# Performance work log

Hardware: AMD Instinct MI355X
Metric: run time of the kernel (lower is better)

## Reference

```python
import jax, jax.numpy as jnp
import numpy as np

DIM = 1024
HEADS = 16
HEAD_DIM = DIM // HEADS
DFF = 4 * DIM
EPS = 1e-6


def _layernorm(x, scale, bias):
    mu = jnp.mean(x, axis=-1, keepdims=True)
    var = jnp.mean(jnp.square(x - mu), axis=-1, keepdims=True)
    return (x - mu) * jax.lax.rsqrt(var + EPS) * scale + bias


def setup_inputs() -> dict:
    key = jax.random.key(0)
    ks = jax.random.split(key, 8)
    d = {}
    d["x"] = jax.random.normal(ks[0], (4, 2048, DIM), dtype=jnp.float32)
    # LayerNorm params
    d["ln1_scale"] = jnp.ones((DIM,), jnp.float32)
    d["ln1_bias"] = jnp.zeros((DIM,), jnp.float32)
    d["ln2_scale"] = jnp.ones((DIM,), jnp.float32)
    d["ln2_bias"] = jnp.zeros((DIM,), jnp.float32)
    # Attention params
    d["qkv_w"] = jax.random.normal(ks[1], (DIM, 3 * DIM), jnp.float32) * (DIM ** -0.5)
    d["qkv_b"] = jnp.zeros((3 * DIM,), jnp.float32)
    d["proj_w"] = jax.random.normal(ks[2], (DIM, DIM), jnp.float32) * (DIM ** -0.5)
    d["proj_b"] = jnp.zeros((DIM,), jnp.float32)
    # MLP params
    d["fc1_w"] = jax.random.normal(ks[3], (DIM, DFF), jnp.float32) * (DIM ** -0.5)
    d["fc1_b"] = jnp.zeros((DFF,), jnp.float32)
    d["fc2_w"] = jax.random.normal(ks[4], (DFF, DIM), jnp.float32) * (DFF ** -0.5)
    d["fc2_b"] = jnp.zeros((DIM,), jnp.float32)
    return d


def reference(x, ln1_scale, ln1_bias, ln2_scale, ln2_bias,
              qkv_w, qkv_b, proj_w, proj_b,
              fc1_w, fc1_b, fc2_w, fc2_b):
    B, S, D = x.shape
    scale = HEAD_DIM ** -0.5

    # --- Attention sub-block (pre-LN) ---
    h = _layernorm(x, ln1_scale, ln1_bias)
    qkv = h @ qkv_w + qkv_b                                  # [B,S,3D]
    qkv = qkv.reshape(B, S, 3, HEADS, HEAD_DIM)
    qkv = qkv.transpose(2, 0, 3, 1, 4)                       # [3,B,H,S,hd]
    q, k, v = qkv[0], qkv[1], qkv[2]
    attn = jnp.einsum('bhqd,bhkd->bhqk', q, k) * scale       # [B,H,S,S]
    attn = jax.nn.softmax(attn, axis=-1)
    out = jnp.einsum('bhqk,bhkd->bhqd', attn, v)             # [B,H,S,hd]
    out = out.transpose(0, 2, 1, 3).reshape(B, S, D)
    out = out @ proj_w + proj_b
    x = x + out

    # --- MLP sub-block (pre-LN) ---
    h = _layernorm(x, ln2_scale, ln2_bias)
    h = jax.nn.gelu(h @ fc1_w + fc1_b)
    h = h @ fc2_w + fc2_b
    return x + h
```

## Files before the change

kernel.cpp:

```cpp
#include <hip/hip_runtime.h>
#include <hip/hip_bf16.h>

typedef __attribute__((ext_vector_type(4))) float f32x4;
typedef __attribute__((ext_vector_type(16))) float f32x16;
typedef __attribute__((ext_vector_type(8))) short bf16x8;

__device__ __forceinline__ unsigned short f2bf(float f) {
    return __bfloat16_as_ushort(__float2bfloat16(f));
}

typedef __attribute__((address_space(1))) const unsigned char* gas_ptr;
typedef __attribute__((address_space(3))) unsigned char* las_ptr;
__device__ __forceinline__ void gload16(const void* g, void* l) {
    __builtin_amdgcn_global_load_lds((gas_ptr)g, (las_ptr)l, 16, 0, 0);
}

__device__ __forceinline__ unsigned cvt_pk_bf16(float lo, float hi) {
    unsigned r;
    asm("v_cvt_pk_bf16_f32 %0, %1, %2" : "=v"(r) : "v"(lo), "v"(hi));
    return r;
}

__global__ __launch_bounds__(256) void ln_kernel(
    const float* __restrict__ x, const float* __restrict__ scale,
    const float* __restrict__ bias, unsigned short* __restrict__ out)
{
    int row = blockIdx.x;
    const float* xr = x + (size_t)row * 1024;
    int t = threadIdx.x;
    float4 v = ((const float4*)xr)[t];
    float s  = v.x + v.y + v.z + v.w;
    float ss = v.x*v.x + v.y*v.y + v.z*v.z + v.w*v.w;
    #pragma unroll
    for (int m = 32; m; m >>= 1) { s += __shfl_down(s, m); ss += __shfl_down(ss, m); }
    __shared__ float red[8];
    int wid = t >> 6;
    if ((t & 63) == 0) { red[wid*2] = s; red[wid*2+1] = ss; }
    __syncthreads();
    s  = red[0] + red[2] + red[4] + red[6];
    ss = red[1] + red[3] + red[5] + red[7];
    float mu  = s * (1.0f/1024.0f);
    float var = ss * (1.0f/1024.0f) - mu*mu;
    float inv = rsqrtf(var + 1e-6f);
    float4 sc = ((const float4*)scale)[t];
    float4 bi = ((const float4*)bias)[t];
    ushort4 o;
    o.x = f2bf((v.x - mu)*inv*sc.x + bi.x);
    o.y = f2bf((v.y - mu)*inv*sc.y + bi.y);
    o.z = f2bf((v.z - mu)*inv*sc.z + bi.z);
    o.w = f2bf((v.w - mu)*inv*sc.w + bi.w);
    ((ushort4*)(out + (size_t)row * 1024))[t] = o;
}

__global__ __launch_bounds__(256) void transpose_kernel(
    const float* __restrict__ W, unsigned short* __restrict__ Wt, int K, int N)
{
    __shared__ float tile[32][33];
    int n0 = blockIdx.x * 32, k0 = blockIdx.y * 32;
    int tx = threadIdx.x, ty = threadIdx.y;
    #pragma unroll
    for (int j = 0; j < 32; j += 8)
        tile[ty + j][tx] = W[(size_t)(k0 + ty + j) * N + n0 + tx];
    __syncthreads();
    #pragma unroll
    for (int j = 0; j < 32; j += 8)
        Wt[(size_t)(n0 + ty + j) * K + k0 + tx] = f2bf(tile[tx][ty + j]);
}

template<int EPI>
__global__ __launch_bounds__(512, 2) void gemm256_kernel(
    const unsigned short* __restrict__ A,
    const unsigned short* __restrict__ Bt,
    const float* __restrict__ bias,
    const float* __restrict__ res,
    void* __restrict__ out,
    unsigned short* __restrict__ vtout,
    int M, int N, int K)
{
    constexpr int BM = 256;
    constexpr int BN = 128;

    __shared__ __align__(16) unsigned short Al[3][BM * 64];
    __shared__ __align__(16) unsigned short Bl[3][BN * 64];

    int t = threadIdx.x;
    int wid = t >> 6, lane = t & 63;
    int wr = wid >> 1, wc = wid & 1;
    int l15 = lane & 15, lg = lane >> 4;

    int gx = gridDim.x;
    int nwg = gx * gridDim.y;
    int orig = blockIdx.y * gx + blockIdx.x;
    int cpx = nwg >> 3;
    int wg = (orig & 7) * cpx + (orig >> 3);
    int bx = wg % gx, by = wg / gx;
    int brow = by * BM, bcol = bx * BN;

    f32x4 acc[4][4] = {};

    int sr  = t >> 3;
    int scb = (t & 7) * 16;
    int sce = (scb ^ ((sr & 7) << 4)) >> 1;
    const size_t aoff = (size_t)(brow + sr) * K + sce;
    const size_t boff = (size_t)(bcol + sr) * K + sce;

    auto stage = [&](int b, int kt2) {
        int k0 = kt2 << 6;
        char* la = (char*)Al[b] + (wid << 10);
        char* lb = (char*)Bl[b] + (wid << 10);
        #pragma unroll
        for (int i = 0; i < 4; i++)
            gload16(A + aoff + (size_t)(i * 64) * K + k0, la + i * 8192);
        #pragma unroll
        for (int j = 0; j < 2; j++)
            gload16(Bt + boff + (size_t)(j * 64) * K + k0, lb + j * 8192);
    };

    int nk = K >> 6;
    stage(0, 0);
    __builtin_amdgcn_sched_barrier(0);
    stage(1, 1);
    asm volatile("s_waitcnt vmcnt(6)" ::: "memory");
    __builtin_amdgcn_s_barrier();

    int rsw = (l15 & 7) << 4;
    int cur = 0, nxt2 = 2;
    for (int kt = 0; kt < nk; kt++) {
        if (kt + 2 < nk) stage(nxt2, kt + 2);

        const char* Ab = (const char*)Al[cur];
        const char* Bb = (const char*)Bl[cur];

        bf16x8 bfr[4][2];
        #pragma unroll
        for (int nf = 0; nf < 4; nf++) {
            int rb = wc * 64 + nf * 16 + l15;
            #pragma unroll
            for (int kk = 0; kk < 2; kk++)
                bfr[nf][kk] = *(const bf16x8*)(Bb + rb * 128 + ((kk * 64 + lg * 16) ^ rsw));
        }
        bf16x8 af[4][2];
        #pragma unroll
        for (int mf = 0; mf < 4; mf++) {
            int ra = wr * 64 + mf * 16 + l15;
            #pragma unroll
            for (int kk = 0; kk < 2; kk++)
                af[mf][kk] = *(const bf16x8*)(Ab + ra * 128 + ((kk * 64 + lg * 16) ^ rsw));
        }
        __builtin_amdgcn_s_setprio(1);
        #pragma unroll
        for (int mf = 0; mf < 4; mf++)
            #pragma unroll
            for (int nf = 0; nf < 4; nf++)
                #pragma unroll
                for (int kk = 0; kk < 2; kk++)
                    acc[mf][nf] = __builtin_amdgcn_mfma_f32_16x16x32_bf16(
                        af[mf][kk], bfr[nf][kk], acc[mf][nf], 0, 0, 0);
        __builtin_amdgcn_s_setprio(0);

        if (kt + 2 < nk)      asm volatile("s_waitcnt vmcnt(6)" ::: "memory");
        else if (kt + 1 < nk) asm volatile("s_waitcnt vmcnt(0)" ::: "memory");
        __builtin_amdgcn_s_barrier();

        cur  = (cur  == 2) ? 0 : cur  + 1;
        nxt2 = (nxt2 == 2) ? 0 : nxt2 + 1;
    }

    #pragma unroll
    for (int mi = 0; mi < 4; mi++) {
        #pragma unroll
        for (int nf = 0; nf < 4; nf++) {
            int col = bcol + wc * 64 + nf * 16 + l15;
            float bs = bias[col];
            #pragma unroll
            for (int r = 0; r < 4; r++) {
                int row = brow + wr * 64 + mi * 16 + lg * 4 + r;
                size_t idx = (size_t)row * N + col;
                float v = acc[mi][nf][r] + bs;
                if (EPI == 1) {
                    ((float*)out)[idx] = v + res[idx];
                } else if (EPI == 2) {
                    float u = v + 0.044715f * v * v * v;
                    float e = __builtin_amdgcn_exp2f(-2.3022077f * u);
                    float g = v * __builtin_amdgcn_rcpf(1.0f + e);
                    ((unsigned short*)out)[idx] = f2bf(g);
                } else {
                    unsigned short bv = f2bf(v);
                    ((unsigned short*)out)[idx] = bv;
                    if (col >= 2048) {
                        int hd = col - 2048;
                        int b = row >> 11, s = row & 2047;
                        vtout[((size_t)((b << 4) + (hd >> 6)) * 64 + (hd & 63)) * 2048 + s] = bv;
                    }
                }
            }
        }
    }
}

__global__ __launch_bounds__(512, 2) void attn_kernel(
    const unsigned short* __restrict__ qkv, const unsigned short* __restrict__ vt,
    unsigned short* __restrict__ ctx)
{
    __shared__ unsigned short Kl[2][4096];
    __shared__ unsigned short Vl[2][4096];

    int t = threadIdx.x;
    int wid = t >> 6, lane = t & 63;
    int l31 = lane & 31, half = lane >> 5;
    int bh = blockIdx.y;
    int b = bh >> 4, h = bh & 15;
    int qr0 = blockIdx.x * 256 + wid * 32;

    const size_t qbase = (size_t)b * 2048 * 3072 + (size_t)h * 64;
    const unsigned short* vbase = vt + (size_t)bh * 64 * 2048;

    bf16x8 qf[4];
    #pragma unroll
    for (int ds = 0; ds < 4; ds++)
        qf[ds] = *(const bf16x8*)(qkv + qbase + (size_t)(qr0 + l31) * 3072 + ds*16 + half*8);

    f32x16 ot0 = {}, ot1 = {};
    float mrun = -1e30f, lrun = 0.0f;
    const float C = 0.125f * 1.44269504f;

    int srow = t >> 3;
    int ssw = ((t & 7) * 16) ^ ((srow & 7) << 4);
    const unsigned short* kg = qkv + qbase + 1024 + (size_t)srow * 3072 + (ssw >> 1);
    const unsigned short* vg = vbase + (size_t)srow * 2048 + (ssw >> 1);

    gload16(kg, (char*)Kl[0] + t * 16);
    gload16(vg, (char*)Vl[0] + t * 16);
    __syncthreads();

    int cur = 0;
    for (int kt = 0; kt < 32; kt++) {
        if (kt < 31) {
            gload16(kg + (size_t)(kt + 1) * 64 * 3072, (char*)Kl[cur ^ 1] + t * 16);
            gload16(vg + (kt + 1) * 64,               (char*)Vl[cur ^ 1] + t * 16);
        }

        const char* Kb = (const char*)Kl[cur];
        const char* Vb = (const char*)Vl[cur];
        int sw = (l31 & 7) << 4;

        f32x16 st0 = {}, st1 = {};
        __builtin_amdgcn_s_setprio(1);
        #pragma unroll
        for (int ds = 0; ds < 4; ds++) {
            int colb = ds*32 + half*16;
            bf16x8 k0 = *(const bf16x8*)(Kb + l31*128 + (colb ^ sw));
            bf16x8 k1 = *(const bf16x8*)(Kb + (32 + l31)*128 + (colb ^ sw));
            st0 = __builtin_amdgcn_mfma_f32_32x32x16_bf16(k0, qf[ds], st0, 0, 0, 0);
            st1 = __builtin_amdgcn_mfma_f32_32x32x16_bf16(k1, qf[ds], st1, 0, 0, 0);
        }
        __builtin_amdgcn_s_setprio(0);

        float mx = fmaxf(st0[0], st0[1]);
        #pragma unroll
        for (int r = 2; r < 16; r++) mx = fmaxf(mx, st0[r]);
        #pragma unroll
        for (int r = 0; r < 16; r++) mx = fmaxf(mx, st1[r]);
        mx = fmaxf(mx, __shfl_xor(mx, 32));
        float pm = mx * C;

        bool grow = pm > mrun + 11.5416f;
        if (__any(grow)) {
            float mn = fmaxf(mrun, pm);
            float corr = __builtin_amdgcn_exp2f(mrun - mn);
            mrun = mn;
            lrun *= corr;
            ot0 *= corr;
            ot1 *= corr;
        }

        unsigned w0[8], w1[8];
        float sum = 0.0f;
        {
            float e[16];
            #pragma unroll
            for (int r = 0; r < 16; r++) { e[r] = __builtin_amdgcn_exp2f(fmaf(st0[r], C, -mrun)); sum += e[r]; }
            #pragma unroll
            for (int p = 0; p < 8; p++) w0[p] = cvt_pk_bf16(e[2*p], e[2*p+1]);
            #pragma unroll
            for (int r = 0; r < 16; r++) { e[r] = __builtin_amdgcn_exp2f(fmaf(st1[r], C, -mrun)); sum += e[r]; }
            #pragma unroll
            for (int p = 0; p < 8; p++) w1[p] = cvt_pk_bf16(e[2*p], e[2*p+1]);
        }
        lrun += sum;

        __builtin_amdgcn_s_setprio(1);
        #pragma unroll
        for (int ks = 0; ks < 4; ks++) {
            union { unsigned u[4]; bf16x8 v; } pf;
            unsigned* w = (ks < 2) ? w0 : w1;
            int o4 = (ks & 1) * 4;
            pf.u[0] = w[o4 + 0]; pf.u[1] = w[o4 + 1]; pf.u[2] = w[o4 + 2]; pf.u[3] = w[o4 + 3];
            int lo = ks*32 + half*8;
            union { unsigned long long d[2]; bf16x8 v; } va, vb;
            va.d[0] = *(const unsigned long long*)(Vb + l31*128 + (lo ^ sw));
            va.d[1] = *(const unsigned long long*)(Vb + l31*128 + ((lo + 16) ^ sw));
            vb.d[0] = *(const unsigned long long*)(Vb + (32 + l31)*128 + (lo ^ sw));
            vb.d[1] = *(const unsigned long long*)(Vb + (32 + l31)*128 + ((lo + 16) ^ sw));
            ot0 = __builtin_amdgcn_mfma_f32_32x32x16_bf16(va.v, pf.v, ot0, 0, 0, 0);
            ot1 = __builtin_amdgcn_mfma_f32_32x32x16_bf16(vb.v, pf.v, ot1, 0, 0, 0);
        }
        __builtin_amdgcn_s_setprio(0);

        __syncthreads();
        cur ^= 1;
    }

    float ltot = lrun + __shfl_xor(lrun, 32);
    float rl = 1.0f / ltot;
    size_t cb = (size_t)b * 2048 * 1024 + (size_t)(qr0 + l31) * 1024 + (size_t)h * 64;
    #pragma unroll
    for (int r = 0; r < 16; r++) {
        int d = (r & 3) + 8 * (r >> 2) + 4 * half;
        ctx[cb + d]      = f2bf(ot0[r] * rl);
        ctx[cb + 32 + d] = f2bf(ot1[r] * rl);
    }
}

extern "C" void kernel_launch(void* const* d_in, const int* in_sizes, int n_in,
                              void* d_out, int out_size, void* d_ws, size_t ws_size,
                              hipStream_t stream) {
    const float* x      = (const float*)d_in[0];
    const float* ln1_s  = (const float*)d_in[1];
    const float* ln1_b  = (const float*)d_in[2];
    const float* ln2_s  = (const float*)d_in[3];
    const float* ln2_b  = (const float*)d_in[4];
    const float* qkv_w  = (const float*)d_in[5];
    const float* qkv_b  = (const float*)d_in[6];
    const float* proj_w = (const float*)d_in[7];
    const float* proj_b = (const float*)d_in[8];
    const float* fc1_w  = (const float*)d_in[9];
    const float* fc1_b  = (const float*)d_in[10];
    const float* fc2_w  = (const float*)d_in[11];
    const float* fc2_b  = (const float*)d_in[12];
    float* out = (float*)d_out;

    char* ws = (char*)d_ws;
    unsigned short* vtb  = (unsigned short*)(ws + 0);
    float*          x1   = (float*)(ws + 0);
    unsigned short* h    = (unsigned short*)(ws + (size_t)32 * 1024 * 1024);
    unsigned short* qkvb = (unsigned short*)(ws + (size_t)48 * 1024 * 1024);
    unsigned short* gbuf = (unsigned short*)(ws + (size_t)48 * 1024 * 1024);
    unsigned short* ctxb = (unsigned short*)(ws + (size_t)96 * 1024 * 1024);
    unsigned short* wT   = (unsigned short*)(ws + (size_t)112 * 1024 * 1024);

    dim3 tb(32, 8);

    transpose_kernel<<<dim3(96, 32), tb, 0, stream>>>(qkv_w, wT, 1024, 3072);
    ln_kernel<<<8192, 256, 0, stream>>>(x, ln1_s, ln1_b, h);
    gemm256_kernel<3><<<dim3(24, 32), 512, 0, stream>>>(h, wT, qkv_b, nullptr, qkvb, vtb, 8192, 3072, 1024);
    attn_kernel<<<dim3(8, 64), 512, 0, stream>>>(qkvb, vtb, ctxb);
    transpose_kernel<<<dim3(32, 32), tb, 0, stream>>>(proj_w, wT, 1024, 1024);
    gemm256_kernel<1><<<dim3(8, 32), 512, 0, stream>>>(ctxb, wT, proj_b, x, x1, nullptr, 8192, 1024, 1024);
    ln_kernel<<<8192, 256, 0, stream>>>(x1, ln2_s, ln2_b, h);
    transpose_kernel<<<dim3(128, 32), tb, 0, stream>>>(fc1_w, wT, 1024, 4096);
    gemm256_kernel<2><<<dim3(32, 32), 512, 0, stream>>>(h, wT, fc1_b, nullptr, gbuf, nullptr, 8192, 4096, 1024);
    transpose_kernel<<<dim3(32, 128), tb, 0, stream>>>(fc2_w, wT, 4096, 1024);
    gemm256_kernel<1><<<dim3(8, 32), 512, 0, stream>>>(gbuf, wT, fc2_b, x1, out, nullptr, 8192, 1024, 4096);
}
```

Baseline: 446.6 us.

## Add 256x256 four-phase pipelined GEMM for QKV and FC1, double-buffer others

Adds a new GEMM kernel with 256x256 tiles that splits each K-step into four MFMA phases. Each phase interleaves LDS fragment reads and global-to-LDS prefetch of the next tile with barriers and priority hints. The QKV and FC1 projections use it, which halves their grid sizes and raises arithmetic intensity per tile. The existing 256x128 kernel drops from triple to double buffering with a full vmcnt(0) wait each iteration. That lowers LDS use but may expose more load latency for the proj and FC2 GEMMs.

```diff
diff --git a/kernel.cpp b/kernel.cpp
--- a/kernel.cpp
+++ b/kernel.cpp
@@ -68,6 +68,191 @@
 }
 
 template<int EPI>
+__global__ __launch_bounds__(512, 2) void gemm4p_kernel(
+    const unsigned short* __restrict__ A,
+    const unsigned short* __restrict__ Bt,
+    const float* __restrict__ bias,
+    const float* __restrict__ res,
+    void* __restrict__ out,
+    unsigned short* __restrict__ vtout,
+    int M, int N, int K)
+{
+    __shared__ __align__(16) unsigned short Al[2][256 * 64];
+    __shared__ __align__(16) unsigned short Bl[2][256 * 64];
+
+    int t = threadIdx.x;
+    int wid = t >> 6, lane = t & 63;
+    int wr = wid >> 2, wc = wid & 3;
+    int l15 = lane & 15, lg = lane >> 4;
+
+    int gx = gridDim.x;
+    int nwg = gx * gridDim.y;
+    int orig = blockIdx.y * gx + blockIdx.x;
+    int cpx = nwg >> 3;
+    int wg = (orig & 7) * cpx + (orig >> 3);
+    int bx = wg % gx, by = wg / gx;
+    int brow = by * 256, bcol = bx * 256;
+
+    f32x4 acc[8][4] = {};
+
+    int sr  = t >> 3;
+    int scb = (t & 7) * 16;
+    int sce = (scb ^ ((sr & 7) << 4)) >> 1;
+    const size_t aoff = (size_t)(brow + sr) * K + sce;
+    const size_t boff = (size_t)(bcol + sr) * K + sce;
+
+    auto stgA = [&](int b, int kt2, int s0, int s1) {
+        int k0 = kt2 << 6;
+        char* la = (char*)Al[b] + (wid << 10);
+        gload16(A + aoff + (size_t)(s0 * 64) * K + k0, la + s0 * 8192);
+        gload16(A + aoff + (size_t)(s1 * 64) * K + k0, la + s1 * 8192);
+    };
+    auto stgB = [&](int b, int kt2, int s0, int s1) {
+        int k0 = kt2 << 6;
+        char* lb = (char*)Bl[b] + (wid << 10);
+        gload16(Bt + boff + (size_t)(s0 * 64) * K + k0, lb + s0 * 8192);
+        gload16(Bt + boff + (size_t)(s1 * 64) * K + k0, lb + s1 * 8192);
+    };
+
+    int nk = K >> 6;
+    stgB(0, 0, 0, 1); stgB(0, 0, 2, 3);
+    stgA(0, 0, 0, 2); stgA(0, 0, 1, 3);
+    asm volatile("s_waitcnt vmcnt(0)" ::: "memory");
+    __builtin_amdgcn_s_barrier();
+
+    int rsw = (l15 & 7) << 4;
+    for (int kt = 0; kt < nk; kt++) {
+        int cur = kt & 1, nxt = cur ^ 1;
+        bool st = (kt + 1 < nk);
+        const char* Ab = (const char*)Al[cur];
+        const char* Bb = (const char*)Bl[cur];
+        bf16x8 bfr[4], af[4];
+
+        #pragma unroll
+        for (int nf = 0; nf < 4; nf++) {
+            int rb = wc * 64 + nf * 16 + l15;
+            bfr[nf] = *(const bf16x8*)(Bb + rb * 128 + ((lg * 16) ^ rsw));
+        }
+        #pragma unroll
+        for (int mf = 0; mf < 4; mf++) {
+            int ra = wr * 128 + mf * 16 + l15;
+            af[mf] = *(const bf16x8*)(Ab + ra * 128 + ((lg * 16) ^ rsw));
+        }
+        if (st) stgB(nxt, kt + 1, 0, 1);
+        if (st) asm volatile("s_waitcnt vmcnt(2)" ::: "memory");
+        else    asm volatile("s_waitcnt vmcnt(0)" ::: "memory");
+        __builtin_amdgcn_sched_barrier(0);
+        __builtin_amdgcn_s_barrier();
+        asm volatile("s_waitcnt lgkmcnt(0)" ::: "memory");
+        __builtin_amdgcn_sched_barrier(0);
+        __builtin_amdgcn_s_setprio(1);
+        #pragma unroll
+        for (int mf = 0; mf < 4; mf++)
+            #pragma unroll
+            for (int nf = 0; nf < 4; nf++)
+                acc[mf][nf] = __builtin_amdgcn_mfma_f32_16x16x32_bf16(af[mf], bfr[nf], acc[mf][nf], 0, 0, 0);
+        __builtin_amdgcn_s_setprio(0);
+        __builtin_amdgcn_s_barrier();
+
+        #pragma unroll
+        for (int mf = 0; mf < 4; mf++) {
+            int ra = wr * 128 + 64 + mf * 16 + l15;
+            af[mf] = *(const bf16x8*)(Ab + ra * 128 + ((lg * 16) ^ rsw));
+        }
+        if (st) stgB(nxt, kt + 1, 2, 3);
+        __builtin_amdgcn_sched_barrier(0);
+        __builtin_amdgcn_s_barrier();
+        asm volatile("s_waitcnt lgkmcnt(0)" ::: "memory");
+        __builtin_amdgcn_sched_barrier(0);
+        __builtin_amdgcn_s_setprio(1);
+        #pragma unroll
+        for (int mf = 0; mf < 4; mf++)
+            #pragma unroll
+            for (int nf = 0; nf < 4; nf++)
+                acc[4 + mf][nf] = __builtin_amdgcn_mfma_f32_16x16x32_bf16(af[mf], bfr[nf], acc[4 + mf][nf], 0, 0, 0);
+        __builtin_amdgcn_s_setprio(0);
+        __builtin_amdgcn_s_barrier();
+
+        #pragma unroll
+        for (int nf = 0; nf < 4; nf++) {
+            int rb = wc * 64 + nf * 16 + l15;
+            bfr[nf] = *(const bf16x8*)(Bb + rb * 128 + ((64 + lg * 16) ^ rsw));
+        }
+        #pragma unroll
+        for (int mf = 0; mf < 4; mf++) {
+            int ra = wr * 128 + mf * 16 + l15;
+            af[mf] = *(const bf16x8*)(Ab + ra * 128 + ((64 + lg * 16) ^ rsw));
+        }
+        if (st) stgA(nxt, kt + 1, 0, 2);
+        __builtin_amdgcn_sched_barrier(0);
+        __builtin_amdgcn_s_barrier();
+        asm volatile("s_waitcnt lgkmcnt(0)" ::: "memory");
+        __builtin_amdgcn_sched_barrier(0);
+        __builtin_amdgcn_s_setprio(1);
+        #pragma unroll
+        for (int mf = 0; mf < 4; mf++)
+            #pragma unroll
+            for (int nf = 0; nf < 4; nf++)
+                acc[mf][nf] = __builtin_amdgcn_mfma_f32_16x16x32_bf16(af[mf], bfr[nf], acc[mf][nf], 0, 0, 0);
+        __builtin_amdgcn_s_setprio(0);
+        __builtin_amdgcn_s_barrier();
+
+        #pragma unroll
+        for (int mf = 0; mf < 4; mf++) {
+            int ra = wr * 128 + 64 + mf * 16 + l15;
+            af[mf] = *(const bf16x8*)(Ab + ra * 128 + ((64 + lg * 16) ^ rsw));
+        }
+        if (st) {
+            stgA(nxt, kt + 1, 1, 3);
+            asm volatile("s_waitcnt vmcnt(2)" ::: "memory");
+        }
+        __builtin_amdgcn_sched_barrier(0);
+        __builtin_amdgcn_s_barrier();
+        asm volatile("s_waitcnt lgkmcnt(0)" ::: "memory");
+        __builtin_amdgcn_sched_barrier(0);
+        __builtin_amdgcn_s_setprio(1);
+        #pragma unroll
+        for (int mf = 0; mf < 4; mf++)
+            #pragma unroll
+            for (int nf = 0; nf < 4; nf++)
+                acc[4 + mf][nf] = __builtin_amdgcn_mfma_f32_16x16x32_bf16(af[mf], bfr[nf], acc[4 + mf][nf], 0, 0, 0);
+        __builtin_amdgcn_s_setprio(0);
+        __builtin_amdgcn_s_barrier();
+    }
+
+    #pragma unroll
+    for (int mi = 0; mi < 8; mi++) {
+        #pragma unroll
+        for (int nf = 0; nf < 4; nf++) {
+            int col = bcol + wc * 64 + nf * 16 + l15;
+            float bs = bias[col];
+            #pragma unroll
+            for (int r = 0; r < 4; r++) {
+                int row = brow + wr * 128 + mi * 16 + lg * 4 + r;
+                size_t idx = (size_t)row * N + col;
+                float v = acc[mi][nf][r] + bs;
+                if (EPI == 1) {
+                    ((float*)out)[idx] = v + res[idx];
+                } else if (EPI == 2) {
+                    float u = v + 0.044715f * v * v * v;
+                    float e = __builtin_amdgcn_exp2f(-2.3022077f * u);
+                    float g = v * __builtin_amdgcn_rcpf(1.0f + e);
+                    ((unsigned short*)out)[idx] = f2bf(g);
+                } else {
+                    unsigned short bv = f2bf(v);
+                    ((unsigned short*)out)[idx] = bv;
+                    if (col >= 2048) {
+                        int hd = col - 2048;
+                        int b = row >> 11, s = row & 2047;
+                        vtout[((size_t)((b << 4) + (hd >> 6)) * 64 + (hd & 63)) * 2048 + s] = bv;
+                    }
+                }
+            }
+        }
+    }
+}
+
+template<int EPI>
 __global__ __launch_bounds__(512, 2) void gemm256_kernel(
     const unsigned short* __restrict__ A,
     const unsigned short* __restrict__ Bt,
@@ -77,11 +262,8 @@
     unsigned short* __restrict__ vtout,
     int M, int N, int K)
 {
-    constexpr int BM = 256;
-    constexpr int BN = 128;
-
-    __shared__ __align__(16) unsigned short Al[3][BM * 64];
-    __shared__ __align__(16) unsigned short Bl[3][BN * 64];
+    __shared__ __align__(16) unsigned short Al[2][256 * 64];
+    __shared__ __align__(16) unsigned short Bl[2][128 * 64];
 
     int t = threadIdx.x;
     int wid = t >> 6, lane = t & 63;
@@ -94,7 +276,7 @@
     int cpx = nwg >> 3;
     int wg = (orig & 7) * cpx + (orig >> 3);
     int bx = wg % gx, by = wg / gx;
-    int brow = by * BM, bcol = bx * BN;
+    int brow = by * 256, bcol = bx * 128;
 
     f32x4 acc[4][4] = {};
 
@@ -116,17 +298,15 @@
             gload16(Bt + boff + (size_t)(j * 64) * K + k0, lb + j * 8192);
     };
 
+    stage(0, 0);
+    asm volatile("s_waitcnt vmcnt(0)" ::: "memory");
+    __builtin_amdgcn_s_barrier();
+
     int nk = K >> 6;
-    stage(0, 0);
-    __builtin_amdgcn_sched_barrier(0);
-    stage(1, 1);
-    asm volatile("s_waitcnt vmcnt(6)" ::: "memory");
-    __builtin_amdgcn_s_barrier();
-
     int rsw = (l15 & 7) << 4;
-    int cur = 0, nxt2 = 2;
     for (int kt = 0; kt < nk; kt++) {
-        if (kt + 2 < nk) stage(nxt2, kt + 2);
+        int cur = kt & 1;
+        if (kt + 1 < nk) stage(cur ^ 1, kt + 1);
 
         const char* Ab = (const char*)Al[cur];
         const char* Bb = (const char*)Bl[cur];
@@ -158,12 +338,8 @@
                         af[mf][kk], bfr[nf][kk], acc[mf][nf], 0, 0, 0);
         __builtin_amdgcn_s_setprio(0);
 
-        if (kt + 2 < nk)      asm volatile("s_waitcnt vmcnt(6)" ::: "memory");
-        else if (kt + 1 < nk) asm volatile("s_waitcnt vmcnt(0)" ::: "memory");
-        __builtin_amdgcn_s_barrier();
-
-        cur  = (cur  == 2) ? 0 : cur  + 1;
-        nxt2 = (nxt2 == 2) ? 0 : nxt2 + 1;
+        asm volatile("s_waitcnt vmcnt(0)" ::: "memory");
+        __builtin_amdgcn_s_barrier();
     }
 
     #pragma unroll
@@ -353,13 +529,13 @@
 
     transpose_kernel<<<dim3(96, 32), tb, 0, stream>>>(qkv_w, wT, 1024, 3072);
     ln_kernel<<<8192, 256, 0, stream>>>(x, ln1_s, ln1_b, h);
-    gemm256_kernel<3><<<dim3(24, 32), 512, 0, stream>>>(h, wT, qkv_b, nullptr, qkvb, vtb, 8192, 3072, 1024);
+    gemm4p_kernel<3><<<dim3(12, 32), 512, 0, stream>>>(h, wT, qkv_b, nullptr, qkvb, vtb, 8192, 3072, 1024);
     attn_kernel<<<dim3(8, 64), 512, 0, stream>>>(qkvb, vtb, ctxb);
     transpose_kernel<<<dim3(32, 32), tb, 0, stream>>>(proj_w, wT, 1024, 1024);
     gemm256_kernel<1><<<dim3(8, 32), 512, 0, stream>>>(ctxb, wT, proj_b, x, x1, nullptr, 8192, 1024, 1024);
     ln_kernel<<<8192, 256, 0, stream>>>(x1, ln2_s, ln2_b, h);
     transpose_kernel<<<dim3(128, 32), tb, 0, stream>>>(fc1_w, wT, 1024, 4096);
-    gemm256_kernel<2><<<dim3(32, 32), 512, 0, stream>>>(h, wT, fc1_b, nullptr, gbuf, nullptr, 8192, 4096, 1024);
+    gemm4p_kernel<2><<<dim3(16, 32), 512, 0, stream>>>(h, wT, fc1_b, nullptr, gbuf, nullptr, 8192, 4096, 1024);
     transpose_kernel<<<dim3(32, 128), tb, 0, stream>>>(fc2_w, wT, 4096, 1024);
     gemm256_kernel<1><<<dim3(8, 32), 512, 0, stream>>>(gbuf, wT, fc2_b, x1, out, nullptr, 8192, 1024, 4096);
 }
```

Result: faster. 416.2 us (-6.8%).

## Replace triple-buffered 256x128 GEMM with single-buffered 128x128 tile kernel

Applied to the files above, without the earlier changes.

Changes the GEMM from 512-thread blocks with 256x128 tiles and a three-stage global-to-LDS pipeline to 256-thread blocks with 128x128 tiles and a single LDS buffer. Each K step now loads, syncs and computes with no prefetch overlap. The aim is higher occupancy (4 blocks per CU) and more blocks to hide latency, in place of software pipelining. The cost is that load latency is exposed behind barriers and operand reuse per tile is lower.

```diff
diff --git a/kernel.cpp b/kernel.cpp
--- a/kernel.cpp
+++ b/kernel.cpp
@@ -68,7 +68,7 @@
 }
 
 template<int EPI>
-__global__ __launch_bounds__(512, 2) void gemm256_kernel(
+__global__ __launch_bounds__(256, 4) void gemm_kernel(
     const unsigned short* __restrict__ A,
     const unsigned short* __restrict__ Bt,
     const float* __restrict__ bias,
@@ -77,11 +77,8 @@
     unsigned short* __restrict__ vtout,
     int M, int N, int K)
 {
-    constexpr int BM = 256;
-    constexpr int BN = 128;
-
-    __shared__ __align__(16) unsigned short Al[3][BM * 64];
-    __shared__ __align__(16) unsigned short Bl[3][BN * 64];
+    __shared__ __align__(16) unsigned short Al[128 * 64];
+    __shared__ __align__(16) unsigned short Bl[128 * 64];
 
     int t = threadIdx.x;
     int wid = t >> 6, lane = t & 63;
@@ -94,7 +91,7 @@
     int cpx = nwg >> 3;
     int wg = (orig & 7) * cpx + (orig >> 3);
     int bx = wg % gx, by = wg / gx;
-    int brow = by * BM, bcol = bx * BN;
+    int brow = by * 128, bcol = bx * 128;
 
     f32x4 acc[4][4] = {};
 
@@ -103,67 +100,38 @@
     int sce = (scb ^ ((sr & 7) << 4)) >> 1;
     const size_t aoff = (size_t)(brow + sr) * K + sce;
     const size_t boff = (size_t)(bcol + sr) * K + sce;
-
-    auto stage = [&](int b, int kt2) {
-        int k0 = kt2 << 6;
-        char* la = (char*)Al[b] + (wid << 10);
-        char* lb = (char*)Bl[b] + (wid << 10);
-        #pragma unroll
-        for (int i = 0; i < 4; i++)
-            gload16(A + aoff + (size_t)(i * 64) * K + k0, la + i * 8192);
-        #pragma unroll
-        for (int j = 0; j < 2; j++)
-            gload16(Bt + boff + (size_t)(j * 64) * K + k0, lb + j * 8192);
-    };
+    char* la = (char*)Al + (wid << 10);
+    char* lb = (char*)Bl + (wid << 10);
 
     int nk = K >> 6;
-    stage(0, 0);
-    __builtin_amdgcn_sched_barrier(0);
-    stage(1, 1);
-    asm volatile("s_waitcnt vmcnt(6)" ::: "memory");
-    __builtin_amdgcn_s_barrier();
-
     int rsw = (l15 & 7) << 4;
-    int cur = 0, nxt2 = 2;
     for (int kt = 0; kt < nk; kt++) {
-        if (kt + 2 < nk) stage(nxt2, kt + 2);
-
-        const char* Ab = (const char*)Al[cur];
-        const char* Bb = (const char*)Bl[cur];
-
-        bf16x8 bfr[4][2];
-        #pragma unroll
-        for (int nf = 0; nf < 4; nf++) {
-            int rb = wc * 64 + nf * 16 + l15;
-            #pragma unroll
-            for (int kk = 0; kk < 2; kk++)
-                bfr[nf][kk] = *(const bf16x8*)(Bb + rb * 128 + ((kk * 64 + lg * 16) ^ rsw));
-        }
-        bf16x8 af[4][2];
-        #pragma unroll
-        for (int mf = 0; mf < 4; mf++) {
-            int ra = wr * 64 + mf * 16 + l15;
-            #pragma unroll
-            for (int kk = 0; kk < 2; kk++)
-                af[mf][kk] = *(const bf16x8*)(Ab + ra * 128 + ((kk * 64 + lg * 16) ^ rsw));
-        }
-        __builtin_amdgcn_s_setprio(1);
-        #pragma unroll
-        for (int mf = 0; mf < 4; mf++)
+        int k0 = kt << 6;
+        __syncthreads();
+        #pragma unroll
+        for (int i = 0; i < 4; i++) {
+            gload16(A  + aoff + (size_t)(i * 32) * K + k0, la + i * 4096);
+            gload16(Bt + boff + (size_t)(i * 32) * K + k0, lb + i * 4096);
+        }
+        __syncthreads();
+        #pragma unroll
+        for (int kf = 0; kf < 2; kf++) {
+            bf16x8 af[4], bfr[4];
+            #pragma unroll
+            for (int mf = 0; mf < 4; mf++)
+                af[mf] = *(const bf16x8*)((const char*)Al + (wr*64 + mf*16 + l15)*128 + ((kf*64 + lg*16) ^ rsw));
             #pragma unroll
             for (int nf = 0; nf < 4; nf++)
+                bfr[nf] = *(const bf16x8*)((const char*)Bl + (wc*64 + nf*16 + l15)*128 + ((kf*64 + lg*16) ^ rsw));
+            __builtin_amdgcn_s_setprio(1);
+            #pragma unroll
+            for (int mf = 0; mf < 4; mf++)
                 #pragma unroll
-                for (int kk = 0; kk < 2; kk++)
+                for (int nf = 0; nf < 4; nf++)
                     acc[mf][nf] = __builtin_amdgcn_mfma_f32_16x16x32_bf16(
-                        af[mf][kk], bfr[nf][kk], acc[mf][nf], 0, 0, 0);
-        __builtin_amdgcn_s_setprio(0);
-
-        if (kt + 2 < nk)      asm volatile("s_waitcnt vmcnt(6)" ::: "memory");
-        else if (kt + 1 < nk) asm volatile("s_waitcnt vmcnt(0)" ::: "memory");
-        __builtin_amdgcn_s_barrier();
-
-        cur  = (cur  == 2) ? 0 : cur  + 1;
-        nxt2 = (nxt2 == 2) ? 0 : nxt2 + 1;
+                        af[mf], bfr[nf], acc[mf][nf], 0, 0, 0);
+            __builtin_amdgcn_s_setprio(0);
+        }
     }
 
     #pragma unroll
@@ -353,13 +321,13 @@
 
     transpose_kernel<<<dim3(96, 32), tb, 0, stream>>>(qkv_w, wT, 1024, 3072);
     ln_kernel<<<8192, 256, 0, stream>>>(x, ln1_s, ln1_b, h);
-    gemm256_kernel<3><<<dim3(24, 32), 512, 0, stream>>>(h, wT, qkv_b, nullptr, qkvb, vtb, 8192, 3072, 1024);
+    gemm_kernel<3><<<dim3(24, 64), 256, 0, stream>>>(h, wT, qkv_b, nullptr, qkvb, vtb, 8192, 3072, 1024);
     attn_kernel<<<dim3(8, 64), 512, 0, stream>>>(qkvb, vtb, ctxb);
     transpose_kernel<<<dim3(32, 32), tb, 0, stream>>>(proj_w, wT, 1024, 1024);
-    gemm256_kernel<1><<<dim3(8, 32), 512, 0, stream>>>(ctxb, wT, proj_b, x, x1, nullptr, 8192, 1024, 1024);
+    gemm_kernel<1><<<dim3(8, 64), 256, 0, stream>>>(ctxb, wT, proj_b, x, x1, nullptr, 8192, 1024, 1024);
     ln_kernel<<<8192, 256, 0, stream>>>(x1, ln2_s, ln2_b, h);
     transpose_kernel<<<dim3(128, 32), tb, 0, stream>>>(fc1_w, wT, 1024, 4096);
-    gemm256_kernel<2><<<dim3(32, 32), 512, 0, stream>>>(h, wT, fc1_b, nullptr, gbuf, nullptr, 8192, 4096, 1024);
+    gemm_kernel<2><<<dim3(32, 64), 256, 0, stream>>>(h, wT, fc1_b, nullptr, gbuf, nullptr, 8192, 4096, 1024);
     transpose_kernel<<<dim3(32, 128), tb, 0, stream>>>(fc2_w, wT, 4096, 1024);
-    gemm256_kernel<1><<<dim3(8, 32), 512, 0, stream>>>(gbuf, wT, fc2_b, x1, out, nullptr, 8192, 1024, 4096);
-}
+    gemm_kernel<1><<<dim3(8, 64), 256, 0, stream>>>(gbuf, wT, fc2_b, x1, out, nullptr, 8192, 1024, 4096);
+}
```

Measured after the change: 396.7 us. 1.13x faster.
